# Performance work log

Measured on AMD Instinct MI355X. Metric: run time of the kernel, lower is better.

## Reference

```python
import jax, jax.numpy as jnp
import numpy as np

B = 256          # batch
MID = 16384      # mid_siz
OUT = 16384      # out_siz
C = 16           # channel_siz
NLVL = 8         # nlvl (== klvl here since floor(log2(OUT/2))=13 >= 8)
MIDF = MID >> NLVL   # mid_filter_siz = 64
OUTF = OUT >> NLVL   # out_filter_siz = 64
NB = 1 << NLVL       # 256 leaf branches
STD = 0.5


def setup_inputs() -> dict:
    key = jax.random.key(0)
    ks = jax.random.split(key, 6)
    in_data = jax.random.normal(ks[0], (B, MID, 2), jnp.float32)
    # learned parameters (buildRand: normal(0, 0.5) filters, zero biases)
    mid_dense = jax.random.normal(ks[1], (1, MID, 2), jnp.float32) * STD
    in_filter = jax.random.normal(ks[2], (MIDF, 1, C), jnp.float32) * STD   # conv1d [width,in,out]
    in_bias = jnp.zeros((C,), jnp.float32)
    # level lvl (1..NLVL) uses filters[lvl-1, :2**lvl]; padded to NB branches
    filters = jax.random.normal(ks[3], (NLVL, NB, 2, C, C), jnp.float32) * STD
    biases = jnp.zeros((NLVL, NB, C), jnp.float32)
    fea_dense = jax.random.normal(ks[4], (NB, C, OUTF), jnp.float32) * STD
    return dict(in_data=in_data, mid_dense=mid_dense, in_filter=in_filter,
                in_bias=in_bias, filters=filters, biases=biases, fea_dense=fea_dense)


def reference(in_data, mid_dense, in_filter, in_bias, filters, biases, fea_dense):
    # elementwise modulation then split real/imag channels: (B, 2, MID)
    x = jnp.moveaxis(in_data * mid_dense, -1, 1)
    # level-0 conv1d: kernel MIDF, stride MIDF//2 -> overlapping half-windows.
    # Split signal into half-width chunks h; window t = [h[t], h[t+1]].
    half = MIDF // 2
    h = x.reshape(B, 2, MID // half, half)                 # (B,2,512,32)
    W1 = in_filter[:half, 0, :]                            # (32,C)
    W2 = in_filter[half:, 0, :]
    s = jnp.einsum('bisw,wc->bisc', h[:, :, :-1], W1) \
        + jnp.einsum('bisw,wc->bisc', h[:, :, 1:], W2)
    s = jax.nn.relu(s + in_bias)                           # (B,2,2^(n+1)-1,C)
    state = s[:, :, None]                                  # (B,2,nb=1,L,C)
    # butterfly tree: each level doubles branches; conv kernel=2, stride=2, VALID
    for lvl in range(1, NLVL + 1):
        nb = 1 << lvl
        p = jnp.repeat(state, 2, axis=2)                   # child itk <- parent itk//2
        L = p.shape[3]                                     # odd: 2^(n+1-lvl+1)-1
        xw = p[:, :, :, :L - 1, :].reshape(B, 2, nb, (L - 1) // 2, 2, C)
        W = filters[lvl - 1, :nb]                          # (nb,2,C,C)
        bb = biases[lvl - 1, :nb]                          # (nb,C)
        state = jax.nn.relu(
            jnp.einsum('bintkc,nkcd->bintd', xw, W) + bb[None, None, :, None, :])
    feat = state[:, :, :, 0, :]                            # (B,2,NB,C): L==1 at last level
    outp = jnp.einsum('binc,ncf->binf', feat, fea_dense)   # per-branch dense projection
    R = outp[:, 0].reshape(B, OUT // 2, 2)
    I = outp[:, 1].reshape(B, OUT // 2, 2)
    out_data = ((R[:, :, 0] - I[:, :, 1]) / MID).reshape(B, OUT // 2, 1)
    return out_data, R[:, :, 1]
```

## Files before the change

### kernel.cpp

```cpp
#include <hip/hip_runtime.h>
#include <hip/hip_bf16.h>


#define OUT_HALF 2097152

typedef __attribute__((ext_vector_type(4))) float f32x4;
typedef __attribute__((ext_vector_type(8))) short s16x8;

__device__ __forceinline__ uint fsw(uint a) {
    return a ^ ((((a >> 6) ^ (a >> 8)) & 3u) << 4);
}
__device__ __forceinline__ ushort bfr(float f) {
    __hip_bfloat16 h = __float2bfloat16(f);
    union { __hip_bfloat16 h; ushort u; } cv; cv.h = h; return cv.u;
}
__device__ __forceinline__ uint pk(float a, float b) {
    return (uint)bfr(a) | ((uint)bfr(b) << 16);
}

__device__ __forceinline__ void tree_level(
    char* smb, const int lane, const int wave,
    uint AOff, uint NOff, int lgR, int lgNP, int nTiles,
    uint WOff, int wnb, uint LBOff, int bnb)
{
    const int m  = lane & 15;
    const int kg = lane >> 4;
    const int lgTPP = lgR - 4;
    for (int at = wave; at < nTiles; at += 4) {
        const int p  = at >> lgTPP;
        const int tc = at & ((1 << lgTPP) - 1);
        const int np = p & ((1 << lgNP) - 1);
        const int ii = p >> lgNP;
        s16x8 af = *(const s16x8*)(smb + AOff + (p << (lgR + 6)) +
                                   fsw((uint)((tc * 16 + m) * 64 + kg * 16)));
#pragma unroll
        for (int sib = 0; sib < 2; sib++) {
            const int nl = 2 * np + sib;
            s16x8 bf = *(const s16x8*)(smb + WOff +
                         fsw((uint)((wnb + nl) * 1024 + m * 64 + kg * 16)));
            float bv = *(const float*)(smb + LBOff + ((bnb + nl) * 16 + m) * 4);
            f32x4 acc = {bv, bv, bv, bv};
            acc = __builtin_amdgcn_mfma_f32_16x16x32_bf16(af, bf, acc, 0, 0, 0);
            const int p2 = (ii << (lgNP + 1)) + nl;
            const uint wb = NOff + (p2 << (lgR + 5));
            const int r2 = tc * 8 + kg * 2;
            *(uint*)(smb + wb + fsw((uint)(r2 * 64 + m * 4))) =
                pk(fmaxf(acc.x, 0.f), fmaxf(acc.y, 0.f));
            *(uint*)(smb + wb + fsw((uint)((r2 + 1) * 64 + m * 4))) =
                pk(fmaxf(acc.z, 0.f), fmaxf(acc.w, 0.f));
        }
    }
}

__global__ __launch_bounds__(256, 3)
void ibf_A(const float* __restrict__ in_data, const float* __restrict__ mid_dense,
           const float* __restrict__ in_filter, const float* __restrict__ in_bias,
           const float* __restrict__ filters, const float* __restrict__ biases,
           uint* __restrict__ S3)
{
    __shared__ __align__(16) char smb[42048];
    const int tid = threadIdx.x, lane = tid & 63, wave = tid >> 6;
    const int b = blockIdx.x, th = blockIdx.y;

    {
        const float4* inb = (const float4*)in_data + (size_t)b * 8192 + th * 2048;
        const float4* mdb = (const float4*)mid_dense + th * 2048;
        for (int mp = tid; mp < 2064; mp += 256) {
            float4 iv = inb[mp], mv = mdb[mp];
            *(uint*)(smb + 0    + fsw((uint)(mp * 4))) = pk(iv.x * mv.x, iv.z * mv.z);
            *(uint*)(smb + 8256 + fsw((uint)(mp * 4))) = pk(iv.y * mv.y, iv.w * mv.w);
        }
    }
    for (int t = tid; t < 3584; t += 256) {
        int nidx = t >> 8, r = t & 255, d = r & 15, c = r >> 4;
        int lvl = (nidx < 2) ? 1 : ((nidx < 6) ? 2 : 3);
        int n = nidx - ((1 << lvl) - 2);
        const float* src = filters + (size_t)(lvl - 1) * 131072 + n * 512 + c * 16 + d;
        *(uint*)(smb + 24704 + fsw((uint)(nidx * 1024 + d * 64 + c * 4))) = pk(src[0], src[256]);
    }
    for (int t = tid; t < 512; t += 256) {
        int c = t >> 5, w2 = t & 31;
        *(uint*)(smb + 39040 + fsw((uint)(c * 128 + w2 * 4))) =
            pk(in_filter[(2 * w2) * 16 + c], in_filter[(2 * w2 + 1) * 16 + c]);
    }
    if (tid < 240) {
        float v;
        if (tid < 224) {
            int nidx = tid >> 4;
            int lvl = (nidx < 2) ? 1 : ((nidx < 6) ? 2 : 3);
            int n = nidx - ((1 << lvl) - 2);
            v = biases[(size_t)(lvl - 1) * 4096 + n * 16 + (tid & 15)];
        } else v = in_bias[tid - 224];
        *(float*)(smb + 41088 + tid * 4) = v;
    }
    __syncthreads();

    {
        const int m = lane & 15, kg = lane >> 4;
        s16x8 b0 = *(const s16x8*)(smb + 39040 + fsw((uint)(m * 128 + kg * 16)));
        s16x8 b1 = *(const s16x8*)(smb + 39040 + fsw((uint)(m * 128 + 64 + kg * 16)));
        float bv = *(const float*)(smb + 41088 + (224 + m) * 4);
        for (int at = wave; at < 16; at += 4) {
            int i = at >> 3, tc = at & 7;
            uint xb = i ? 8256u : 0u;
            s16x8 a0 = *(const s16x8*)(smb + xb + fsw((uint)((tc * 16 + m) * 64 + kg * 16)));
            s16x8 a1 = *(const s16x8*)(smb + xb + fsw((uint)((tc * 16 + m) * 64 + 64 + kg * 16)));
            f32x4 acc = {bv, bv, bv, bv};
            acc = __builtin_amdgcn_mfma_f32_16x16x32_bf16(a0, b0, acc, 0, 0, 0);
            acc = __builtin_amdgcn_mfma_f32_16x16x32_bf16(a1, b1, acc, 0, 0, 0);
            uint wb = 16512u + (uint)i * 4096u;
            int r2 = tc * 8 + kg * 2;
            *(uint*)(smb + wb + fsw((uint)(r2 * 64 + m * 4))) =
                pk(fmaxf(acc.x, 0.f), fmaxf(acc.y, 0.f));
            *(uint*)(smb + wb + fsw((uint)((r2 + 1) * 64 + m * 4))) =
                pk(fmaxf(acc.z, 0.f), fmaxf(acc.w, 0.f));
        }
    }
    __syncthreads();
    tree_level(smb, lane, wave, 16512, 0,    6, 0, 8, 24704, 0, 41088, 0);
    __syncthreads();
    tree_level(smb, lane, wave, 0,     8256, 5, 1, 8, 24704, 2, 41088, 2);
    __syncthreads();
    {
        const int m = lane & 63 & 15, kg = (lane & 63) >> 4;
        for (int at = wave; at < 8; at += 4) {
            int np = at & 3, i = at >> 2;
            s16x8 af = *(const s16x8*)(smb + 8256 + (at << 10) + fsw((uint)(m * 64 + kg * 16)));
#pragma unroll
            for (int sib = 0; sib < 2; sib++) {
                int n3 = 2 * np + sib;
                s16x8 bf = *(const s16x8*)(smb + 24704 +
                             fsw((uint)((6 + n3) * 1024 + m * 64 + kg * 16)));
                float bv = *(const float*)(smb + 41088 + ((6 + n3) * 16 + m) * 4);
                f32x4 acc = {bv, bv, bv, bv};
                acc = __builtin_amdgcn_mfma_f32_16x16x32_bf16(af, bf, acc, 0, 0, 0);
                int bi = 2 * b + i;
                int t4 = th * 8 + kg * 2;
                uint idx = ((uint)(n3 * 512 + bi) * 16 + t4) * 16 + m;
                S3[idx]      = pk(fmaxf(acc.x, 0.f), fmaxf(acc.y, 0.f));
                S3[idx + 16] = pk(fmaxf(acc.z, 0.f), fmaxf(acc.w, 0.f));
            }
        }
    }
}

__global__ __launch_bounds__(256, 2)
void ibf_B(const float* __restrict__ filters, const float* __restrict__ biases,
           const uint* __restrict__ S3, char* __restrict__ S8)
{
    __shared__ __align__(16) char smb[61312];
    const int tid = threadIdx.x, lane = tid & 63, wave = tid >> 6;
    const int n3 = blockIdx.x, chunk = blockIdx.y;

    {
        const char* src = (const char*)S3 + ((size_t)n3 * 512 + chunk * 8) * 1024;
        for (int ci = tid; ci < 512; ci += 256)
            *(float4*)(smb + fsw((uint)(ci * 16))) = *(const float4*)(src + ci * 16);
    }
    for (int t = tid; t < 992; t += 256) {
        int nidx = t >> 4, q = nidx + 2;
        int l3 = 31 - __clz(q);
        int nl = q - (1 << l3);
        int gn = (n3 << l3) + nl;
        *(float*)(smb + 57344 + t * 4) = biases[(size_t)(l3 + 2) * 4096 + gn * 16 + (t & 15)];
    }
    auto stage_w = [&](int l3) {
        int NL = 1 << l3;
        const float* fb = filters + (size_t)(l3 + 2) * 131072;
        for (int t = tid; t < NL * 256; t += 256) {
            int nl = t >> 8, r = t & 255, d = r & 15, c = r >> 4;
            const float* src = fb + (size_t)((n3 << l3) + nl) * 512 + c * 16 + d;
            *(uint*)(smb + 24576 + fsw((uint)(nl * 1024 + d * 64 + c * 4))) = pk(src[0], src[256]);
        }
    };
    stage_w(1);
    __syncthreads();
    tree_level(smb, lane, wave, 0,    8192, 7, 0, 8, 24576, 0, 57344, 0);
    __syncthreads();
    stage_w(2);
    __syncthreads();
    tree_level(smb, lane, wave, 8192, 0,    6, 1, 8, 24576, 0, 57344, 2);
    __syncthreads();
    stage_w(3);
    __syncthreads();
    tree_level(smb, lane, wave, 0,    8192, 5, 2, 8, 24576, 0, 57344, 6);
    __syncthreads();
    stage_w(4);
    __syncthreads();
    tree_level(smb, lane, wave, 8192, 0,    4, 3, 8, 24576, 0, 57344, 14);
    __syncthreads();
    stage_w(5);
    __syncthreads();
    {
        const int m = lane & 15, kg = lane >> 4;
        for (int at = wave; at < 16; at += 4) {
            s16x8 af = *(const s16x8*)(smb + at * 512 + fsw((uint)(m * 64 + kg * 16)));
#pragma unroll
            for (int sib = 0; sib < 2; sib++) {
                int nl = 2 * at + sib;
                s16x8 bf = *(const s16x8*)(smb + 24576 +
                             fsw((uint)(nl * 1024 + m * 64 + kg * 16)));
                float bv = *(const float*)(smb + 57344 + ((30 + nl) * 16 + m) * 4);
                f32x4 acc = {bv, bv, bv, bv};
                acc = __builtin_amdgcn_mfma_f32_16x16x32_bf16(af, bf, acc, 0, 0, 0);
                if (kg < 2) {
                    float v[4] = {fmaxf(acc.x, 0.f), fmaxf(acc.y, 0.f),
                                  fmaxf(acc.z, 0.f), fmaxf(acc.w, 0.f)};
#pragma unroll
                    for (int j = 0; j < 4; j++)
                        *(ushort*)(smb + 16384 + nl * 256 + (kg * 4 + j) * 32 + m * 2) = bfr(v[j]);
                }
            }
        }
    }
    __syncthreads();
    {
        float4* dst = (float4*)(S8 + (size_t)(n3 * 64 + chunk) * 8192);
        for (int ci = tid; ci < 512; ci += 256)
            dst[ci] = *(const float4*)(smb + 16384 + ci * 16);
    }
}

__global__ __launch_bounds__(128, 8)
void ibf_C(const float* __restrict__ fea_dense, const char* __restrict__ S8,
           float* __restrict__ out)
{
    __shared__ ushort FEb[1024];
    const int tid = threadIdx.x, lane = tid & 63, wave = tid >> 6;
    const int n8g = blockIdx.x, half = blockIdx.y;
    const int n3 = n8g >> 5, n8l = n8g & 31;

    for (int idx = tid; idx < 1024; idx += 128) {
        int c = idx >> 6, u = idx & 63;
        FEb[u * 16 + c] = bfr(fea_dense[(size_t)n8g * 1024 + idx]);
    }
    __syncthreads();

    const int m = lane & 15, kg = lane >> 4;
    s16x8 bfrg[4];
#pragma unroll
    for (int ut = 0; ut < 4; ut++) {
        if (kg < 2) bfrg[ut] = *(const s16x8*)(FEb + (ut * 16 + m) * 16 + kg * 8);
        else        bfrg[ut] = (s16x8){0, 0, 0, 0, 0, 0, 0, 0};
    }
    for (int w8 = 0; w8 < 8; w8++) {
        const int tile  = half * 16 + wave * 8 + w8;
        const int birow = tile * 16 + m;
        s16x8 af = {0, 0, 0, 0, 0, 0, 0, 0};
        if (kg < 2)
            af = *(const s16x8*)(S8 + ((size_t)(n3 * 64 + (birow >> 3)) * 32 + n8l) * 256
                                 + (birow & 7) * 32 + kg * 16);
        const int b0  = (tile * 16 + kg * 4) >> 1;
        const bool odd = (m & 1);
#pragma unroll
        for (int ut = 0; ut < 4; ut++) {
            f32x4 acc = {0.f, 0.f, 0.f, 0.f};
            acc = __builtin_amdgcn_mfma_f32_16x16x32_bf16(af, bfrg[ut], acc, 0, 0, 0);
            float sy = __shfl_xor(acc.y, 1);
            float sw = __shfl_xor(acc.w, 1);
            const int g = n8g * 32 + ut * 8 + (m >> 1);
            float v0 = odd ? acc.x : (acc.x - sy) * (1.f / 16384.f);
            float v1 = odd ? acc.z : (acc.z - sw) * (1.f / 16384.f);
            size_t off = (odd ? (size_t)OUT_HALF : (size_t)0) + (size_t)g;
            out[(size_t)b0 * 8192 + off]       = v0;
            out[(size_t)(b0 + 1) * 8192 + off] = v1;
        }
    }
}

extern "C" void kernel_launch(void* const* d_in, const int* in_sizes, int n_in,
                              void* d_out, int out_size, void* d_ws, size_t ws_size,
                              hipStream_t stream) {
    const float* in_data   = (const float*)d_in[0];
    const float* mid_dense = (const float*)d_in[1];
    const float* in_filter = (const float*)d_in[2];
    const float* in_bias   = (const float*)d_in[3];
    const float* filters   = (const float*)d_in[4];
    const float* biases    = (const float*)d_in[5];
    const float* fea_dense = (const float*)d_in[6];
    float* out = (float*)d_out;
    uint* S3   = (uint*)d_ws;
    char* S8   = (char*)d_ws + (4 << 20);

    ibf_A<<<dim3(256, 2), 256, 0, stream>>>(in_data, mid_dense, in_filter, in_bias,
                                            filters, biases, S3);
    ibf_B<<<dim3(8, 64), 256, 0, stream>>>(filters, biases, S3, S8);
    ibf_C<<<dim3(256, 2), 128, 0, stream>>>(fea_dense, S8, out);
}
```

Before: 40.63 us.

## Fuse three kernels into one persistent kernel with atomic grid barriers

Merges the three stage kernels into a single 512-block launch, using global atomic counters with spin-waits as grid-wide barriers between stages. It also adds a memset to reset the counters before each launch. The aim is to remove the per-kernel launch and drain gaps between the short stages. In exchange it relies on all 512 blocks being co-resident (256 CUs × 2 blocks), which risks deadlock if occupancy drops, and stage A now runs at the lower occupancy bound set for stage B.

```diff
diff --git a/kernel.cpp b/kernel.cpp
--- a/kernel.cpp
+++ b/kernel.cpp
@@ -16,6 +16,18 @@
 }
 __device__ __forceinline__ uint pk(float a, float b) {
     return (uint)bfr(a) | ((uint)bfr(b) << 16);
+}
+
+__device__ __forceinline__ void gsync(uint* ctr) {
+    __syncthreads();
+    if (threadIdx.x == 0) {
+        __threadfence();
+        __hip_atomic_fetch_add(ctr, 1u, __ATOMIC_ACQ_REL, __HIP_MEMORY_SCOPE_AGENT);
+        while (__hip_atomic_load(ctr, __ATOMIC_ACQUIRE, __HIP_MEMORY_SCOPE_AGENT) < 512u)
+            __builtin_amdgcn_s_sleep(2);
+        __threadfence();
+    }
+    __syncthreads();
 }
 
 __device__ __forceinline__ void tree_level(
@@ -52,218 +64,219 @@
     }
 }
 
-__global__ __launch_bounds__(256, 3)
-void ibf_A(const float* __restrict__ in_data, const float* __restrict__ mid_dense,
-           const float* __restrict__ in_filter, const float* __restrict__ in_bias,
-           const float* __restrict__ filters, const float* __restrict__ biases,
-           uint* __restrict__ S3)
-{
-    __shared__ __align__(16) char smb[42048];
-    const int tid = threadIdx.x, lane = tid & 63, wave = tid >> 6;
-    const int b = blockIdx.x, th = blockIdx.y;
-
-    {
-        const float4* inb = (const float4*)in_data + (size_t)b * 8192 + th * 2048;
-        const float4* mdb = (const float4*)mid_dense + th * 2048;
-        for (int mp = tid; mp < 2064; mp += 256) {
-            float4 iv = inb[mp], mv = mdb[mp];
-            *(uint*)(smb + 0    + fsw((uint)(mp * 4))) = pk(iv.x * mv.x, iv.z * mv.z);
-            *(uint*)(smb + 8256 + fsw((uint)(mp * 4))) = pk(iv.y * mv.y, iv.w * mv.w);
-        }
-    }
-    for (int t = tid; t < 3584; t += 256) {
-        int nidx = t >> 8, r = t & 255, d = r & 15, c = r >> 4;
-        int lvl = (nidx < 2) ? 1 : ((nidx < 6) ? 2 : 3);
-        int n = nidx - ((1 << lvl) - 2);
-        const float* src = filters + (size_t)(lvl - 1) * 131072 + n * 512 + c * 16 + d;
-        *(uint*)(smb + 24704 + fsw((uint)(nidx * 1024 + d * 64 + c * 4))) = pk(src[0], src[256]);
-    }
-    for (int t = tid; t < 512; t += 256) {
-        int c = t >> 5, w2 = t & 31;
-        *(uint*)(smb + 39040 + fsw((uint)(c * 128 + w2 * 4))) =
-            pk(in_filter[(2 * w2) * 16 + c], in_filter[(2 * w2 + 1) * 16 + c]);
-    }
-    if (tid < 240) {
-        float v;
-        if (tid < 224) {
-            int nidx = tid >> 4;
-            int lvl = (nidx < 2) ? 1 : ((nidx < 6) ? 2 : 3);
-            int n = nidx - ((1 << lvl) - 2);
-            v = biases[(size_t)(lvl - 1) * 4096 + n * 16 + (tid & 15)];
-        } else v = in_bias[tid - 224];
-        *(float*)(smb + 41088 + tid * 4) = v;
-    }
-    __syncthreads();
-
-    {
-        const int m = lane & 15, kg = lane >> 4;
-        s16x8 b0 = *(const s16x8*)(smb + 39040 + fsw((uint)(m * 128 + kg * 16)));
-        s16x8 b1 = *(const s16x8*)(smb + 39040 + fsw((uint)(m * 128 + 64 + kg * 16)));
-        float bv = *(const float*)(smb + 41088 + (224 + m) * 4);
-        for (int at = wave; at < 16; at += 4) {
-            int i = at >> 3, tc = at & 7;
-            uint xb = i ? 8256u : 0u;
-            s16x8 a0 = *(const s16x8*)(smb + xb + fsw((uint)((tc * 16 + m) * 64 + kg * 16)));
-            s16x8 a1 = *(const s16x8*)(smb + xb + fsw((uint)((tc * 16 + m) * 64 + 64 + kg * 16)));
-            f32x4 acc = {bv, bv, bv, bv};
-            acc = __builtin_amdgcn_mfma_f32_16x16x32_bf16(a0, b0, acc, 0, 0, 0);
-            acc = __builtin_amdgcn_mfma_f32_16x16x32_bf16(a1, b1, acc, 0, 0, 0);
-            uint wb = 16512u + (uint)i * 4096u;
-            int r2 = tc * 8 + kg * 2;
-            *(uint*)(smb + wb + fsw((uint)(r2 * 64 + m * 4))) =
-                pk(fmaxf(acc.x, 0.f), fmaxf(acc.y, 0.f));
-            *(uint*)(smb + wb + fsw((uint)((r2 + 1) * 64 + m * 4))) =
-                pk(fmaxf(acc.z, 0.f), fmaxf(acc.w, 0.f));
-        }
-    }
-    __syncthreads();
-    tree_level(smb, lane, wave, 16512, 0,    6, 0, 8, 24704, 0, 41088, 0);
-    __syncthreads();
-    tree_level(smb, lane, wave, 0,     8256, 5, 1, 8, 24704, 2, 41088, 2);
-    __syncthreads();
-    {
-        const int m = lane & 63 & 15, kg = (lane & 63) >> 4;
-        for (int at = wave; at < 8; at += 4) {
-            int np = at & 3, i = at >> 2;
-            s16x8 af = *(const s16x8*)(smb + 8256 + (at << 10) + fsw((uint)(m * 64 + kg * 16)));
-#pragma unroll
-            for (int sib = 0; sib < 2; sib++) {
-                int n3 = 2 * np + sib;
-                s16x8 bf = *(const s16x8*)(smb + 24704 +
-                             fsw((uint)((6 + n3) * 1024 + m * 64 + kg * 16)));
-                float bv = *(const float*)(smb + 41088 + ((6 + n3) * 16 + m) * 4);
-                f32x4 acc = {bv, bv, bv, bv};
-                acc = __builtin_amdgcn_mfma_f32_16x16x32_bf16(af, bf, acc, 0, 0, 0);
-                int bi = 2 * b + i;
-                int t4 = th * 8 + kg * 2;
-                uint idx = ((uint)(n3 * 512 + bi) * 16 + t4) * 16 + m;
-                S3[idx]      = pk(fmaxf(acc.x, 0.f), fmaxf(acc.y, 0.f));
-                S3[idx + 16] = pk(fmaxf(acc.z, 0.f), fmaxf(acc.w, 0.f));
-            }
-        }
-    }
-}
-
 __global__ __launch_bounds__(256, 2)
-void ibf_B(const float* __restrict__ filters, const float* __restrict__ biases,
-           const uint* __restrict__ S3, char* __restrict__ S8)
+void ibf_fused(const float* __restrict__ in_data, const float* __restrict__ mid_dense,
+               const float* __restrict__ in_filter, const float* __restrict__ in_bias,
+               const float* __restrict__ filters, const float* __restrict__ biases,
+               const float* __restrict__ fea_dense,
+               uint* __restrict__ S3, char* __restrict__ S8, uint* __restrict__ ctrs,
+               float* __restrict__ out)
 {
     __shared__ __align__(16) char smb[61312];
     const int tid = threadIdx.x, lane = tid & 63, wave = tid >> 6;
-    const int n3 = blockIdx.x, chunk = blockIdx.y;
+    const int w = blockIdx.x;
 
     {
-        const char* src = (const char*)S3 + ((size_t)n3 * 512 + chunk * 8) * 1024;
-        for (int ci = tid; ci < 512; ci += 256)
-            *(float4*)(smb + fsw((uint)(ci * 16))) = *(const float4*)(src + ci * 16);
-    }
-    for (int t = tid; t < 992; t += 256) {
-        int nidx = t >> 4, q = nidx + 2;
-        int l3 = 31 - __clz(q);
-        int nl = q - (1 << l3);
-        int gn = (n3 << l3) + nl;
-        *(float*)(smb + 57344 + t * 4) = biases[(size_t)(l3 + 2) * 4096 + gn * 16 + (t & 15)];
-    }
-    auto stage_w = [&](int l3) {
-        int NL = 1 << l3;
-        const float* fb = filters + (size_t)(l3 + 2) * 131072;
-        for (int t = tid; t < NL * 256; t += 256) {
-            int nl = t >> 8, r = t & 255, d = r & 15, c = r >> 4;
-            const float* src = fb + (size_t)((n3 << l3) + nl) * 512 + c * 16 + d;
-            *(uint*)(smb + 24576 + fsw((uint)(nl * 1024 + d * 64 + c * 4))) = pk(src[0], src[256]);
-        }
-    };
-    stage_w(1);
-    __syncthreads();
-    tree_level(smb, lane, wave, 0,    8192, 7, 0, 8, 24576, 0, 57344, 0);
-    __syncthreads();
-    stage_w(2);
-    __syncthreads();
-    tree_level(smb, lane, wave, 8192, 0,    6, 1, 8, 24576, 0, 57344, 2);
-    __syncthreads();
-    stage_w(3);
-    __syncthreads();
-    tree_level(smb, lane, wave, 0,    8192, 5, 2, 8, 24576, 0, 57344, 6);
-    __syncthreads();
-    stage_w(4);
-    __syncthreads();
-    tree_level(smb, lane, wave, 8192, 0,    4, 3, 8, 24576, 0, 57344, 14);
-    __syncthreads();
-    stage_w(5);
-    __syncthreads();
+        const int b = w >> 1, th = w & 1;
+        {
+            const float4* inb = (const float4*)in_data + (size_t)b * 8192 + th * 2048;
+            const float4* mdb = (const float4*)mid_dense + th * 2048;
+            for (int mp = tid; mp < 2064; mp += 256) {
+                float4 iv = inb[mp], mv = mdb[mp];
+                *(uint*)(smb + 0    + fsw((uint)(mp * 4))) = pk(iv.x * mv.x, iv.z * mv.z);
+                *(uint*)(smb + 8256 + fsw((uint)(mp * 4))) = pk(iv.y * mv.y, iv.w * mv.w);
+            }
+        }
+        for (int t = tid; t < 3584; t += 256) {
+            int nidx = t >> 8, r = t & 255, d = r & 15, c = r >> 4;
+            int lvl = (nidx < 2) ? 1 : ((nidx < 6) ? 2 : 3);
+            int n = nidx - ((1 << lvl) - 2);
+            const float* src = filters + (size_t)(lvl - 1) * 131072 + n * 512 + c * 16 + d;
+            *(uint*)(smb + 24704 + fsw((uint)(nidx * 1024 + d * 64 + c * 4))) = pk(src[0], src[256]);
+        }
+        for (int t = tid; t < 512; t += 256) {
+            int c = t >> 5, w2 = t & 31;
+            *(uint*)(smb + 39040 + fsw((uint)(c * 128 + w2 * 4))) =
+                pk(in_filter[(2 * w2) * 16 + c], in_filter[(2 * w2 + 1) * 16 + c]);
+        }
+        if (tid < 240) {
+            float v;
+            if (tid < 224) {
+                int nidx = tid >> 4;
+                int lvl = (nidx < 2) ? 1 : ((nidx < 6) ? 2 : 3);
+                int n = nidx - ((1 << lvl) - 2);
+                v = biases[(size_t)(lvl - 1) * 4096 + n * 16 + (tid & 15)];
+            } else v = in_bias[tid - 224];
+            *(float*)(smb + 41088 + tid * 4) = v;
+        }
+        __syncthreads();
+
+        {
+            const int m = lane & 15, kg = lane >> 4;
+            s16x8 b0 = *(const s16x8*)(smb + 39040 + fsw((uint)(m * 128 + kg * 16)));
+            s16x8 b1 = *(const s16x8*)(smb + 39040 + fsw((uint)(m * 128 + 64 + kg * 16)));
+            float bv = *(const float*)(smb + 41088 + (224 + m) * 4);
+            for (int at = wave; at < 16; at += 4) {
+                int i = at >> 3, tc = at & 7;
+                uint xb = i ? 8256u : 0u;
+                s16x8 a0 = *(const s16x8*)(smb + xb + fsw((uint)((tc * 16 + m) * 64 + kg * 16)));
+                s16x8 a1 = *(const s16x8*)(smb + xb + fsw((uint)((tc * 16 + m) * 64 + 64 + kg * 16)));
+                f32x4 acc = {bv, bv, bv, bv};
+                acc = __builtin_amdgcn_mfma_f32_16x16x32_bf16(a0, b0, acc, 0, 0, 0);
+                acc = __builtin_amdgcn_mfma_f32_16x16x32_bf16(a1, b1, acc, 0, 0, 0);
+                uint wb = 16512u + (uint)i * 4096u;
+                int r2 = tc * 8 + kg * 2;
+                *(uint*)(smb + wb + fsw((uint)(r2 * 64 + m * 4))) =
+                    pk(fmaxf(acc.x, 0.f), fmaxf(acc.y, 0.f));
+                *(uint*)(smb + wb + fsw((uint)((r2 + 1) * 64 + m * 4))) =
+                    pk(fmaxf(acc.z, 0.f), fmaxf(acc.w, 0.f));
+            }
+        }
+        __syncthreads();
+        tree_level(smb, lane, wave, 16512, 0,    6, 0, 8, 24704, 0, 41088, 0);
+        __syncthreads();
+        tree_level(smb, lane, wave, 0,     8256, 5, 1, 8, 24704, 2, 41088, 2);
+        __syncthreads();
+        {
+            const int m = lane & 15, kg = lane >> 4;
+            for (int at = wave; at < 8; at += 4) {
+                int np = at & 3, i = at >> 2;
+                s16x8 af = *(const s16x8*)(smb + 8256 + (at << 10) + fsw((uint)(m * 64 + kg * 16)));
+#pragma unroll
+                for (int sib = 0; sib < 2; sib++) {
+                    int n3 = 2 * np + sib;
+                    s16x8 bf = *(const s16x8*)(smb + 24704 +
+                                 fsw((uint)((6 + n3) * 1024 + m * 64 + kg * 16)));
+                    float bv = *(const float*)(smb + 41088 + ((6 + n3) * 16 + m) * 4);
+                    f32x4 acc = {bv, bv, bv, bv};
+                    acc = __builtin_amdgcn_mfma_f32_16x16x32_bf16(af, bf, acc, 0, 0, 0);
+                    int bi = 2 * b + i;
+                    int t4 = th * 8 + kg * 2;
+                    uint idx = ((uint)(n3 * 512 + bi) * 16 + t4) * 16 + m;
+                    S3[idx]      = pk(fmaxf(acc.x, 0.f), fmaxf(acc.y, 0.f));
+                    S3[idx + 16] = pk(fmaxf(acc.z, 0.f), fmaxf(acc.w, 0.f));
+                }
+            }
+        }
+    }
+    gsync(ctrs + 0);
+
     {
+        const int n3 = w & 7, chunk = w >> 3;
+        {
+            const char* src = (const char*)S3 + ((size_t)n3 * 512 + chunk * 8) * 1024;
+            for (int ci = tid; ci < 512; ci += 256)
+                *(float4*)(smb + fsw((uint)(ci * 16))) = *(const float4*)(src + ci * 16);
+        }
+        for (int t = tid; t < 992; t += 256) {
+            int nidx = t >> 4, q = nidx + 2;
+            int l3 = 31 - __clz(q);
+            int nl = q - (1 << l3);
+            int gn = (n3 << l3) + nl;
+            *(float*)(smb + 57344 + t * 4) = biases[(size_t)(l3 + 2) * 4096 + gn * 16 + (t & 15)];
+        }
+        auto stage_w = [&](int l3) {
+            int NL = 1 << l3;
+            const float* fb = filters + (size_t)(l3 + 2) * 131072;
+            for (int t = tid; t < NL * 256; t += 256) {
+                int nl = t >> 8, r = t & 255, d = r & 15, c = r >> 4;
+                const float* src = fb + (size_t)((n3 << l3) + nl) * 512 + c * 16 + d;
+                *(uint*)(smb + 24576 + fsw((uint)(nl * 1024 + d * 64 + c * 4))) = pk(src[0], src[256]);
+            }
+        };
+        stage_w(1);
+        __syncthreads();
+        tree_level(smb, lane, wave, 0,    8192, 7, 0, 8, 24576, 0, 57344, 0);
+        __syncthreads();
+        stage_w(2);
+        __syncthreads();
+        tree_level(smb, lane, wave, 8192, 0,    6, 1, 8, 24576, 0, 57344, 2);
+        __syncthreads();
+        stage_w(3);
+        __syncthreads();
+        tree_level(smb, lane, wave, 0,    8192, 5, 2, 8, 24576, 0, 57344, 6);
+        __syncthreads();
+        stage_w(4);
+        __syncthreads();
+        tree_level(smb, lane, wave, 8192, 0,    4, 3, 8, 24576, 0, 57344, 14);
+        __syncthreads();
+        stage_w(5);
+        __syncthreads();
+        {
+            const int m = lane & 15, kg = lane >> 4;
+            for (int at = wave; at < 16; at += 4) {
+                s16x8 af = *(const s16x8*)(smb + at * 512 + fsw((uint)(m * 64 + kg * 16)));
+#pragma unroll
+                for (int sib = 0; sib < 2; sib++) {
+                    int nl = 2 * at + sib;
+                    s16x8 bf = *(const s16x8*)(smb + 24576 +
+                                 fsw((uint)(nl * 1024 + m * 64 + kg * 16)));
+                    float bv = *(const float*)(smb + 57344 + ((30 + nl) * 16 + m) * 4);
+                    f32x4 acc = {bv, bv, bv, bv};
+                    acc = __builtin_amdgcn_mfma_f32_16x16x32_bf16(af, bf, acc, 0, 0, 0);
+                    if (kg < 2) {
+                        float v[4] = {fmaxf(acc.x, 0.f), fmaxf(acc.y, 0.f),
+                                      fmaxf(acc.z, 0.f), fmaxf(acc.w, 0.f)};
+#pragma unroll
+                        for (int j = 0; j < 4; j++)
+                            *(ushort*)(smb + 16384 + nl * 256 + (kg * 4 + j) * 32 + m * 2) = bfr(v[j]);
+                    }
+                }
+            }
+        }
+        __syncthreads();
+        {
+            float4* dst = (float4*)(S8 + (size_t)(n3 * 64 + chunk) * 8192);
+            for (int ci = tid; ci < 512; ci += 256)
+                dst[ci] = *(const float4*)(smb + 16384 + ci * 16);
+        }
+    }
+    gsync(ctrs + 64);
+
+    {
+        ushort* FEb = (ushort*)smb;
+        const int n8g = w >> 1, qh = w & 1;
+        const int n3 = n8g >> 5, n8l = n8g & 31;
+
+        for (int idx = tid; idx < 1024; idx += 256) {
+            int c = idx >> 6, u = idx & 63;
+            FEb[u * 16 + c] = bfr(fea_dense[(size_t)n8g * 1024 + idx]);
+        }
+        __syncthreads();
+
         const int m = lane & 15, kg = lane >> 4;
-        for (int at = wave; at < 16; at += 4) {
-            s16x8 af = *(const s16x8*)(smb + at * 512 + fsw((uint)(m * 64 + kg * 16)));
-#pragma unroll
-            for (int sib = 0; sib < 2; sib++) {
-                int nl = 2 * at + sib;
-                s16x8 bf = *(const s16x8*)(smb + 24576 +
-                             fsw((uint)(nl * 1024 + m * 64 + kg * 16)));
-                float bv = *(const float*)(smb + 57344 + ((30 + nl) * 16 + m) * 4);
-                f32x4 acc = {bv, bv, bv, bv};
-                acc = __builtin_amdgcn_mfma_f32_16x16x32_bf16(af, bf, acc, 0, 0, 0);
-                if (kg < 2) {
-                    float v[4] = {fmaxf(acc.x, 0.f), fmaxf(acc.y, 0.f),
-                                  fmaxf(acc.z, 0.f), fmaxf(acc.w, 0.f)};
-#pragma unroll
-                    for (int j = 0; j < 4; j++)
-                        *(ushort*)(smb + 16384 + nl * 256 + (kg * 4 + j) * 32 + m * 2) = bfr(v[j]);
+        s16x8 bfrg[4];
+#pragma unroll
+        for (int ut = 0; ut < 4; ut++) {
+            if (kg < 2) bfrg[ut] = *(const s16x8*)(FEb + (ut * 16 + m) * 16 + kg * 8);
+            else        bfrg[ut] = (s16x8){0, 0, 0, 0, 0, 0, 0, 0};
+        }
+#pragma unroll
+        for (int q2 = 0; q2 < 2; q2++) {
+            const int q = qh * 2 + q2;
+            for (int w_ = 0; w_ < 2; w_++) {
+                const int tile  = q * 8 + wave * 2 + w_;
+                const int birow = tile * 16 + m;
+                s16x8 af = {0, 0, 0, 0, 0, 0, 0, 0};
+                if (kg < 2)
+                    af = *(const s16x8*)(S8 + ((size_t)(n3 * 64 + (birow >> 3)) * 32 + n8l) * 256
+                                         + (birow & 7) * 32 + kg * 16);
+                const int b0  = (tile * 16 + kg * 4) >> 1;
+                const bool odd = (m & 1);
+#pragma unroll
+                for (int ut = 0; ut < 4; ut++) {
+                    f32x4 acc = {0.f, 0.f, 0.f, 0.f};
+                    acc = __builtin_amdgcn_mfma_f32_16x16x32_bf16(af, bfrg[ut], acc, 0, 0, 0);
+                    float sy = __shfl_xor(acc.y, 1);
+                    float sw = __shfl_xor(acc.w, 1);
+                    const int g = n8g * 32 + ut * 8 + (m >> 1);
+                    float v0 = odd ? acc.x : (acc.x - sy) * (1.f / 16384.f);
+                    float v1 = odd ? acc.z : (acc.z - sw) * (1.f / 16384.f);
+                    size_t off = (odd ? (size_t)OUT_HALF : (size_t)0) + (size_t)g;
+                    out[(size_t)b0 * 8192 + off]       = v0;
+                    out[(size_t)(b0 + 1) * 8192 + off] = v1;
                 }
             }
-        }
-    }
-    __syncthreads();
-    {
-        float4* dst = (float4*)(S8 + (size_t)(n3 * 64 + chunk) * 8192);
-        for (int ci = tid; ci < 512; ci += 256)
-            dst[ci] = *(const float4*)(smb + 16384 + ci * 16);
-    }
-}
-
-__global__ __launch_bounds__(128, 8)
-void ibf_C(const float* __restrict__ fea_dense, const char* __restrict__ S8,
-           float* __restrict__ out)
-{
-    __shared__ ushort FEb[1024];
-    const int tid = threadIdx.x, lane = tid & 63, wave = tid >> 6;
-    const int n8g = blockIdx.x, half = blockIdx.y;
-    const int n3 = n8g >> 5, n8l = n8g & 31;
-
-    for (int idx = tid; idx < 1024; idx += 128) {
-        int c = idx >> 6, u = idx & 63;
-        FEb[u * 16 + c] = bfr(fea_dense[(size_t)n8g * 1024 + idx]);
-    }
-    __syncthreads();
-
-    const int m = lane & 15, kg = lane >> 4;
-    s16x8 bfrg[4];
-#pragma unroll
-    for (int ut = 0; ut < 4; ut++) {
-        if (kg < 2) bfrg[ut] = *(const s16x8*)(FEb + (ut * 16 + m) * 16 + kg * 8);
-        else        bfrg[ut] = (s16x8){0, 0, 0, 0, 0, 0, 0, 0};
-    }
-    for (int w8 = 0; w8 < 8; w8++) {
-        const int tile  = half * 16 + wave * 8 + w8;
-        const int birow = tile * 16 + m;
-        s16x8 af = {0, 0, 0, 0, 0, 0, 0, 0};
-        if (kg < 2)
-            af = *(const s16x8*)(S8 + ((size_t)(n3 * 64 + (birow >> 3)) * 32 + n8l) * 256
-                                 + (birow & 7) * 32 + kg * 16);
-        const int b0  = (tile * 16 + kg * 4) >> 1;
-        const bool odd = (m & 1);
-#pragma unroll
-        for (int ut = 0; ut < 4; ut++) {
-            f32x4 acc = {0.f, 0.f, 0.f, 0.f};
-            acc = __builtin_amdgcn_mfma_f32_16x16x32_bf16(af, bfrg[ut], acc, 0, 0, 0);
-            float sy = __shfl_xor(acc.y, 1);
-            float sw = __shfl_xor(acc.w, 1);
-            const int g = n8g * 32 + ut * 8 + (m >> 1);
-            float v0 = odd ? acc.x : (acc.x - sy) * (1.f / 16384.f);
-            float v1 = odd ? acc.z : (acc.z - sw) * (1.f / 16384.f);
-            size_t off = (odd ? (size_t)OUT_HALF : (size_t)0) + (size_t)g;
-            out[(size_t)b0 * 8192 + off]       = v0;
-            out[(size_t)(b0 + 1) * 8192 + off] = v1;
         }
     }
 }
@@ -281,9 +294,9 @@
     float* out = (float*)d_out;
     uint* S3   = (uint*)d_ws;
     char* S8   = (char*)d_ws + (4 << 20);
-
-    ibf_A<<<dim3(256, 2), 256, 0, stream>>>(in_data, mid_dense, in_filter, in_bias,
-                                            filters, biases, S3);
-    ibf_B<<<dim3(8, 64), 256, 0, stream>>>(filters, biases, S3, S8);
-    ibf_C<<<dim3(256, 2), 128, 0, stream>>>(fea_dense, S8, out);
-}
+    uint* ctrs = (uint*)((char*)d_ws + (8 << 20));
+
+    hipMemsetAsync(ctrs, 0, 512, stream);
+    ibf_fused<<<512, 256, 0, stream>>>(in_data, mid_dense, in_filter, in_bias,
+                                       filters, biases, fea_dense, S3, S8, ctrs, out);
+}
```

New measurement: 141.6 us. 249% more time.
